# Optimization experiments

Hardware: AMD Instinct MI355X
Metric: run time of the kernel (lower is better)

The kernel has to match this reference:

```python
import jax, jax.numpy as jnp
import numpy as np

B, S, DM, H = 4, 2048, 512, 8
DEPTH = DM // H  # 64


def setup_inputs() -> dict:
    key = jax.random.key(0)
    ks = jax.random.split(key, 12)
    sd = 1.0 / np.sqrt(DM)
    return {
        "Q": jax.random.normal(ks[0], (B, S, DM), jnp.float32),
        "K": jax.random.normal(ks[1], (B, S, DM), jnp.float32),
        "V": jax.random.normal(ks[2], (B, S, DM), jnp.float32),
        "mask": jnp.zeros((B, 1, S), jnp.float32),
        "Wq": jax.random.normal(ks[3], (DM, DM), jnp.float32) * sd,
        "bq": jnp.zeros((DM,), jnp.float32),
        "Wk": jax.random.normal(ks[4], (DM, DM), jnp.float32) * sd,
        "bk": jnp.zeros((DM,), jnp.float32),
        "Wv": jax.random.normal(ks[5], (DM, DM), jnp.float32) * sd,
        "bv": jnp.zeros((DM,), jnp.float32),
        "Wo": jax.random.normal(ks[6], (DM, DM), jnp.float32) * sd,
        "bo": jnp.zeros((DM,), jnp.float32),
    }


def reference(Q, K, V, mask, Wq, bq, Wk, bk, Wv, bv, Wo, bo):
    # Linear projections to [B, S, DM]
    q = Q @ Wq + bq
    k = K @ Wk + bk
    v = V @ Wv + bv
    # Contiguous channel slices of size depth == reshape to [B, S, H, depth]
    q = q.reshape(B, S, H, DEPTH).transpose(0, 2, 1, 3)  # [B,H,S,d]
    k = k.reshape(B, S, H, DEPTH).transpose(0, 2, 1, 3)
    v = v.reshape(B, S, H, DEPTH).transpose(0, 2, 1, 3)
    scale = 1.0 / jnp.sqrt(jnp.asarray(DEPTH, q.dtype))
    scores = jnp.einsum("bhqd,bhkd->bhqk", q, k) * scale  # [B,H,S,S]
    # mask [B,1,S] broadcasts over heads and query positions
    scores = scores + mask[:, None, :, :] * -1e9
    att_ws = jax.nn.softmax(scores, axis=-1)  # [B,H,S,S]
    ctx = jnp.einsum("bhqk,bhkd->bhqd", att_ws, v)  # [B,H,S,d]
    ctx = ctx.transpose(0, 2, 1, 3).reshape(B, S, DM)  # concat heads
    Y = ctx @ Wo + bo
    return Y, att_ws
```

## Files before the change

### kernel.cpp

```cpp
#include <hip/hip_runtime.h>


typedef __bf16 bf16;
typedef __bf16 bf16x8 __attribute__((ext_vector_type(8)));
typedef float f32x4 __attribute__((ext_vector_type(4)));

constexpr int BATCH = 4;
constexpr int SEQ = 2048;
constexpr int DMODEL = 512;
constexpr int NHEAD = 8;
constexpr int HDIM = 64;
constexpr int MTOT = BATCH * SEQ;
constexpr long YELEMS = (long)MTOT * DMODEL;
constexpr long WELEMS = (long)DMODEL * DMODEL;

__device__ __forceinline__ f32x4 mfma_bf16(bf16x8 a, bf16x8 b, f32x4 c) {
  return __builtin_amdgcn_mfma_f32_16x16x32_bf16(a, b, c, 0, 0, 0);
}

__global__ void detect_k(const unsigned int* q, int* flag) {
  unsigned u = q[threadIdx.x];
  int e = (u >> 7) & 0xff;
  unsigned long long m = __ballot(e >= 0x60 && e <= 0x9f);
  if (threadIdx.x == 0) flag[0] = (__popcll(m) >= 48) ? 1 : 0;
}

__global__ void cvt_k(const void* src, bf16* dst, int n, const int* flag) {
  int i = blockIdx.x * 256 + threadIdx.x;
  if (i >= n) return;
  dst[i] = (*flag) ? ((const bf16*)src)[i] : (bf16)((const float*)src)[i];
}

__global__ __launch_bounds__(256) void transpose_w_k(const void* __restrict__ w,
                                                     bf16* __restrict__ wt,
                                                     const int* flag) {
  __shared__ bf16 t[32][33];
  const int f = *flag;
  const int bx = blockIdx.x * 32, by = blockIdx.y * 32;
  const int tx = threadIdx.x & 31, ty = threadIdx.x >> 5;
  for (int i = ty; i < 32; i += 8) {
    const long idx = (long)(by + i) * DMODEL + bx + tx;
    t[i][tx] = f ? ((const bf16*)w)[idx] : (bf16)((const float*)w)[idx];
  }
  __syncthreads();
  for (int i = ty; i < 32; i += 8)
    wt[(long)(bx + i) * DMODEL + by + tx] = t[tx][i];
}

__device__ __forceinline__ void ld8_f32(bf16* dst, const float* p) {
  float4 a = *(const float4*)p;
  float4 b = *(const float4*)(p + 4);
  bf16x8 v;
  v[0] = (bf16)a.x; v[1] = (bf16)a.y; v[2] = (bf16)a.z; v[3] = (bf16)a.w;
  v[4] = (bf16)b.x; v[5] = (bf16)b.y; v[6] = (bf16)b.z; v[7] = (bf16)b.w;
  *(bf16x8*)dst = v;
}

__global__ __launch_bounds__(256) void proj_gemm(
    const void* __restrict__ X, const bf16* __restrict__ Wt,
    const bf16* __restrict__ bias, void* __restrict__ out, int mode, int x_raw,
    const int* flag) {
  __shared__ __attribute__((aligned(16))) bf16 As[64][72];
  __shared__ __attribute__((aligned(16))) bf16 Bs[64][72];
  const int f = *flag;
  const int xf = x_raw ? f : 1;
  const int r0 = blockIdx.x * 64;
  const int c0 = blockIdx.y * 64;
  const int tid = threadIdx.x;
  const int wave = tid >> 6, lane = tid & 63;
  const int quad = lane >> 4, l16 = lane & 15;
  const int srow = tid >> 3, scb = (tid & 7) * 8;

  f32x4 acc[4] = {};
  for (int k0 = 0; k0 < DMODEL; k0 += 64) {
    __syncthreads();
    const long xi0 = (long)(r0 + srow) * DMODEL + k0 + scb;
    const long xi1 = (long)(r0 + srow + 32) * DMODEL + k0 + scb;
    if (xf) {
      *(uint4*)&As[srow][scb] = *(const uint4*)((const bf16*)X + xi0);
      *(uint4*)&As[srow + 32][scb] = *(const uint4*)((const bf16*)X + xi1);
    } else {
      ld8_f32(&As[srow][scb], (const float*)X + xi0);
      ld8_f32(&As[srow + 32][scb], (const float*)X + xi1);
    }
    *(uint4*)&Bs[srow][scb] =
        *(const uint4*)(Wt + (long)(c0 + srow) * DMODEL + k0 + scb);
    *(uint4*)&Bs[srow + 32][scb] =
        *(const uint4*)(Wt + (long)(c0 + srow + 32) * DMODEL + k0 + scb);
    __syncthreads();
    const int m = wave * 16 + l16;
#pragma unroll
    for (int kk = 0; kk < 64; kk += 32) {
      bf16x8 a = *(const bf16x8*)&As[m][kk + quad * 8];
#pragma unroll
      for (int n = 0; n < 4; n++) {
        bf16x8 bb8 = *(const bf16x8*)&Bs[n * 16 + l16][kk + quad * 8];
        acc[n] = mfma_bf16(a, bb8, acc[n]);
      }
    }
  }

  __syncthreads();
  const bool f32out = (mode == 0) && !f;
#pragma unroll
  for (int n = 0; n < 4; n++) {
    const float bvv = (float)bias[c0 + n * 16 + l16];
#pragma unroll
    for (int r = 0; r < 4; r++) {
      const float v = acc[n][r] + bvv;
      const int ml = wave * 16 + quad * 4 + r;
      const int nl = n * 16 + l16;
      if (f32out) {
        ((float*)out)[(long)(r0 + ml) * DMODEL + c0 + nl] = v;
      } else if (mode == 2) {
        As[nl][ml] = (bf16)v;
      } else {
        As[ml][nl] = (bf16)v;
      }
    }
  }
  if (f32out) return;
  __syncthreads();

  const int rb = r0 >> 11;
  const int s0 = r0 & (SEQ - 1);
  const int hh = c0 >> 6;
  bf16* ob = (bf16*)out;
#pragma unroll
  for (int i = 0; i < 2; i++) {
    const int mrow = srow + i * 32;
    long idx;
    if (mode == 0) {
      idx = (long)(r0 + mrow) * DMODEL + c0 + scb;
    } else if (mode == 1) {
      idx = (((long)(rb * NHEAD + hh) * SEQ) + s0 + mrow) * HDIM + scb;
    } else {
      idx = (((long)(rb * NHEAD + hh) * HDIM) + mrow) * SEQ + s0 + scb;
    }
    *(uint4*)(ob + idx) = *(const uint4*)&As[mrow][scb];
  }
}

__global__ __launch_bounds__(256) void attn_k(
    const bf16* __restrict__ qh, const bf16* __restrict__ kh,
    const bf16* __restrict__ vt, const bf16* __restrict__ mask_c,
    bf16* __restrict__ attB, float* __restrict__ attF, bf16* __restrict__ ctx,
    const int* flag) {
  __shared__ __attribute__((aligned(16))) bf16 qs[64][72];
  __shared__ __attribute__((aligned(16))) bf16 ks[64][72];
  __shared__ __attribute__((aligned(16))) bf16 vs[64][72];
  __shared__ __attribute__((aligned(16))) bf16 ps[64][72];
  __shared__ float mk[64];

  const int f = *flag;
  const int bh = blockIdx.y;
  const int bb = bh >> 3, hh = bh & 7;
  const int q0 = blockIdx.x * 64;
  const int tid = threadIdx.x;
  const int wave = tid >> 6, lane = tid & 63;
  const int quad = lane >> 4, l16 = lane & 15;
  const int srow = tid >> 3, scb = (tid & 7) * 8;
  const float scale = 0.125f;

  const bf16* qp = qh + ((long)bh * SEQ + q0) * HDIM;
  const bf16* kp = kh + (long)bh * SEQ * HDIM;
  const bf16* vp = vt + (long)bh * HDIM * SEQ;
  const bf16* mp = mask_c + (long)bb * SEQ;

  *(uint4*)&qs[srow][scb] = *(const uint4*)(qp + (long)srow * HDIM + scb);
  *(uint4*)&qs[srow + 32][scb] =
      *(const uint4*)(qp + (long)(srow + 32) * HDIM + scb);

  float m_ln[4], l_ln[4];
#pragma unroll
  for (int r = 0; r < 4; r++) { m_ln[r] = -3e38f; l_ln[r] = 0.f; }
  const int mrow = wave * 16 + l16;

  for (int t = 0; t < SEQ / 64; t++) {
    __syncthreads();
    const bf16* kt = kp + (long)t * 64 * HDIM;
    *(uint4*)&ks[srow][scb] = *(const uint4*)(kt + (long)srow * HDIM + scb);
    *(uint4*)&ks[srow + 32][scb] =
        *(const uint4*)(kt + (long)(srow + 32) * HDIM + scb);
    if (tid < 64) mk[tid] = -1e9f * (float)mp[t * 64 + tid];
    __syncthreads();
    f32x4 sc[4] = {};
#pragma unroll
    for (int kk = 0; kk < 64; kk += 32) {
      bf16x8 a = *(const bf16x8*)&qs[mrow][kk + quad * 8];
#pragma unroll
      for (int n = 0; n < 4; n++) {
        bf16x8 bb8 = *(const bf16x8*)&ks[n * 16 + l16][kk + quad * 8];
        sc[n] = mfma_bf16(a, bb8, sc[n]);
      }
    }
    float mv[4];
#pragma unroll
    for (int n = 0; n < 4; n++) mv[n] = mk[n * 16 + l16];
#pragma unroll
    for (int r = 0; r < 4; r++) {
      const float v0 = sc[0][r] * scale + mv[0];
      const float v1 = sc[1][r] * scale + mv[1];
      const float v2 = sc[2][r] * scale + mv[2];
      const float v3 = sc[3][r] * scale + mv[3];
      const float mx = fmaxf(fmaxf(v0, v1), fmaxf(v2, v3));
      const float mnew = fmaxf(m_ln[r], mx);
      l_ln[r] = l_ln[r] * __expf(m_ln[r] - mnew) + __expf(v0 - mnew) +
                __expf(v1 - mnew) + __expf(v2 - mnew) + __expf(v3 - mnew);
      m_ln[r] = mnew;
    }
  }

  float m_i[4], rcl[4];
#pragma unroll
  for (int r = 0; r < 4; r++) {
    float mr = m_ln[r];
#pragma unroll
    for (int o = 1; o < 16; o <<= 1) mr = fmaxf(mr, __shfl_xor(mr, o, 64));
    float lr = l_ln[r] * __expf(m_ln[r] - mr);
#pragma unroll
    for (int o = 1; o < 16; o <<= 1) lr += __shfl_xor(lr, o, 64);
    m_i[r] = mr;
    rcl[r] = 1.f / lr;
  }

  f32x4 oacc[4] = {};
  const long abase = ((long)bh * SEQ + q0) * SEQ;

  for (int t = 0; t < SEQ / 64; t++) {
    __syncthreads();
    const bf16* kt = kp + (long)t * 64 * HDIM;
    *(uint4*)&ks[srow][scb] = *(const uint4*)(kt + (long)srow * HDIM + scb);
    *(uint4*)&ks[srow + 32][scb] =
        *(const uint4*)(kt + (long)(srow + 32) * HDIM + scb);
    *(uint4*)&vs[srow][scb] =
        *(const uint4*)(vp + (long)srow * SEQ + t * 64 + scb);
    *(uint4*)&vs[srow + 32][scb] =
        *(const uint4*)(vp + (long)(srow + 32) * SEQ + t * 64 + scb);
    if (tid < 64) mk[tid] = -1e9f * (float)mp[t * 64 + tid];
    __syncthreads();
    f32x4 sc[4] = {};
#pragma unroll
    for (int kk = 0; kk < 64; kk += 32) {
      bf16x8 a = *(const bf16x8*)&qs[mrow][kk + quad * 8];
#pragma unroll
      for (int n = 0; n < 4; n++) {
        bf16x8 bb8 = *(const bf16x8*)&ks[n * 16 + l16][kk + quad * 8];
        sc[n] = mfma_bf16(a, bb8, sc[n]);
      }
    }
    float mv[4];
#pragma unroll
    for (int n = 0; n < 4; n++) mv[n] = mk[n * 16 + l16];
#pragma unroll
    for (int r = 0; r < 4; r++) {
      const int prow = wave * 16 + quad * 4 + r;
#pragma unroll
      for (int n = 0; n < 4; n++) {
        const float p = __expf(sc[n][r] * scale + mv[n] - m_i[r]) * rcl[r];
        ps[prow][n * 16 + l16] = (bf16)p;
        if (!f) attF[abase + (long)prow * SEQ + t * 64 + n * 16 + l16] = p;
      }
    }
    __syncthreads();
#pragma unroll
    for (int kk = 0; kk < 64; kk += 32) {
      bf16x8 a = *(const bf16x8*)&ps[wave * 16 + l16][kk + quad * 8];
#pragma unroll
      for (int n = 0; n < 4; n++) {
        bf16x8 bb8 = *(const bf16x8*)&vs[n * 16 + l16][kk + quad * 8];
        oacc[n] = mfma_bf16(a, bb8, oacc[n]);
      }
    }
    if (f) {
#pragma unroll
      for (int i = 0; i < 2; i++) {
        const int ci = lane + i * 64;
        const int rr = ci >> 3, cc = (ci & 7) * 8;
        *(uint4*)(attB + abase + (long)(wave * 16 + rr) * SEQ + t * 64 + cc) =
            *(const uint4*)&ps[wave * 16 + rr][cc];
      }
    }
  }

#pragma unroll
  for (int n = 0; n < 4; n++) {
#pragma unroll
    for (int r = 0; r < 4; r++) {
      const int s = q0 + wave * 16 + quad * 4 + r;
      const int d = n * 16 + l16;
      ctx[((long)bb * SEQ + s) * DMODEL + hh * HDIM + d] = (bf16)oacc[n][r];
    }
  }
}

extern "C" void kernel_launch(void* const* d_in, const int* in_sizes, int n_in,
                              void* d_out, int out_size, void* d_ws,
                              size_t ws_size, hipStream_t stream) {
  const void* Q = d_in[0];
  const void* K = d_in[1];
  const void* V = d_in[2];
  const void* mask = d_in[3];
  const void* Wq = d_in[4];
  const void* bq = d_in[5];
  const void* Wk = d_in[6];
  const void* bk = d_in[7];
  const void* Wv = d_in[8];
  const void* bv = d_in[9];
  const void* Wo = d_in[10];
  const void* bo = d_in[11];

  char* ob = (char*)d_out;
  bf16* attB = (bf16*)(ob + 2 * YELEMS);
  float* attF = (float*)(ob + 4 * YELEMS);
  bf16* qh = (bf16*)ob;

  bf16* stg = (bf16*)(ob + 4 * YELEMS);
  bf16* wqt = stg;
  bf16* wkt = wqt + WELEMS;
  bf16* wvt = wkt + WELEMS;

  char* wb = (char*)d_ws;
  int* flag = (int*)wb;
  bf16* mask_c = (bf16*)(wb + 16);
  bf16* bq_c = (bf16*)(wb + 16 + 16384);
  bf16* bk_c = bq_c + 512;
  bf16* bv_c = bk_c + 512;
  bf16* bo_c = bv_c + 512;
  bf16* kh = (bf16*)(wb + 20496);
  bf16* vtb = kh + YELEMS;
  bf16* ctx = vtb + YELEMS;
  bf16* wot = ctx + YELEMS;

  dim3 tb(256);
  detect_k<<<1, 64, 0, stream>>>((const unsigned int*)Q, flag);

  cvt_k<<<32, 256, 0, stream>>>(mask, mask_c, BATCH * SEQ, flag);
  cvt_k<<<2, 256, 0, stream>>>(bq, bq_c, DMODEL, flag);
  cvt_k<<<2, 256, 0, stream>>>(bk, bk_c, DMODEL, flag);
  cvt_k<<<2, 256, 0, stream>>>(bv, bv_c, DMODEL, flag);
  cvt_k<<<2, 256, 0, stream>>>(bo, bo_c, DMODEL, flag);

  dim3 gw(DMODEL / 32, DMODEL / 32);
  transpose_w_k<<<gw, tb, 0, stream>>>(Wq, wqt, flag);
  transpose_w_k<<<gw, tb, 0, stream>>>(Wk, wkt, flag);
  transpose_w_k<<<gw, tb, 0, stream>>>(Wv, wvt, flag);
  transpose_w_k<<<gw, tb, 0, stream>>>(Wo, wot, flag);

  dim3 gp(MTOT / 64, DMODEL / 64);
  proj_gemm<<<gp, tb, 0, stream>>>(Q, wqt, bq_c, qh, 1, 1, flag);
  proj_gemm<<<gp, tb, 0, stream>>>(K, wkt, bk_c, kh, 1, 1, flag);
  proj_gemm<<<gp, tb, 0, stream>>>(V, wvt, bv_c, vtb, 2, 1, flag);

  attn_k<<<dim3(SEQ / 64, BATCH * NHEAD), tb, 0, stream>>>(
      qh, kh, vtb, mask_c, attB, attF, ctx, flag);

  proj_gemm<<<gp, tb, 0, stream>>>(ctx, wot, bo_c, d_out, 0, 0, flag);
}
```

Before: 781.9 us.

## Batch small prep kernels, pre-convert QKV to bf16, use exp2 softmax with float mask

Merges the mask and bias conversions into one launch and the four weight transposes into one 3D-grid launch, cutting launch count. Q/K/V are converted to bf16 up front in a separate kernel so the projection GEMM always loads bf16 and drops its per-tile float conversion branch. The attention softmax now uses exp2f with log2e folded into the scale and into a precomputed float mask. Mask values are read per lane from global memory instead of through shared memory. The extra conversion pass adds a full read and write of the inputs, and the bf16 staging buffers are placed inside the output region.

```diff
diff --git a/kernel.cpp b/kernel.cpp
--- a/kernel.cpp
+++ b/kernel.cpp
@@ -13,6 +13,7 @@
 constexpr int MTOT = BATCH * SEQ;
 constexpr long YELEMS = (long)MTOT * DMODEL;
 constexpr long WELEMS = (long)DMODEL * DMODEL;
+constexpr float LOG2E = 1.44269504f;
 
 __device__ __forceinline__ f32x4 mfma_bf16(bf16x8 a, bf16x8 b, f32x4 c) {
   return __builtin_amdgcn_mfma_f32_16x16x32_bf16(a, b, c, 0, 0, 0);
@@ -25,16 +26,57 @@
   if (threadIdx.x == 0) flag[0] = (__popcll(m) >= 48) ? 1 : 0;
 }
 
-__global__ void cvt_k(const void* src, bf16* dst, int n, const int* flag) {
-  int i = blockIdx.x * 256 + threadIdx.x;
-  if (i >= n) return;
-  dst[i] = (*flag) ? ((const bf16*)src)[i] : (bf16)((const float*)src)[i];
-}
-
-__global__ __launch_bounds__(256) void transpose_w_k(const void* __restrict__ w,
-                                                     bf16* __restrict__ wt,
-                                                     const int* flag) {
+__global__ __launch_bounds__(256) void cvt_qkv_k(
+    const void* __restrict__ q, const void* __restrict__ k,
+    const void* __restrict__ v, bf16* __restrict__ qb, bf16* __restrict__ kb,
+    bf16* __restrict__ vb, const int* flag) {
+  const int z = blockIdx.y;
+  const void* src = (z == 0) ? q : (z == 1) ? k : v;
+  bf16* dst = (z == 0) ? qb : (z == 1) ? kb : vb;
+  const long i8 = ((long)blockIdx.x * 256 + threadIdx.x) * 8;
+  if (*flag) {
+    *(uint4*)(dst + i8) = *(const uint4*)((const bf16*)src + i8);
+  } else {
+    const float* s = (const float*)src + i8;
+    const float4 a = *(const float4*)s;
+    const float4 b = *(const float4*)(s + 4);
+    bf16x8 o;
+    o[0] = (bf16)a.x; o[1] = (bf16)a.y; o[2] = (bf16)a.z; o[3] = (bf16)a.w;
+    o[4] = (bf16)b.x; o[5] = (bf16)b.y; o[6] = (bf16)b.z; o[7] = (bf16)b.w;
+    *(bf16x8*)(dst + i8) = o;
+  }
+}
+
+__global__ void cvt_mb_k(const void* __restrict__ mask,
+                         const void* __restrict__ b0,
+                         const void* __restrict__ b1,
+                         const void* __restrict__ b2,
+                         const void* __restrict__ b3,
+                         float* __restrict__ maskf, bf16* __restrict__ bias_c,
+                         const int* flag) {
+  const int f = *flag;
+  const int i = blockIdx.x * 256 + threadIdx.x;
+  if (i < BATCH * SEQ) {
+    const float m = f ? (float)((const bf16*)mask)[i] : ((const float*)mask)[i];
+    maskf[i] = m * (-1e9f * LOG2E);
+  } else {
+    const int j = i - BATCH * SEQ;
+    const int w = j >> 9;
+    const void* s = (w == 0) ? b0 : (w == 1) ? b1 : (w == 2) ? b2 : b3;
+    const int o = j & 511;
+    bias_c[j] = f ? ((const bf16*)s)[o] : (bf16)((const float*)s)[o];
+  }
+}
+
+__global__ __launch_bounds__(256) void transpose_w4_k(
+    const void* __restrict__ wq, const void* __restrict__ wk,
+    const void* __restrict__ wv, const void* __restrict__ wo,
+    bf16* __restrict__ wqt, bf16* __restrict__ wkt, bf16* __restrict__ wvt,
+    bf16* __restrict__ wot, const int* flag) {
   __shared__ bf16 t[32][33];
+  const int z = blockIdx.z;
+  const void* w = (z == 0) ? wq : (z == 1) ? wk : (z == 2) ? wv : wo;
+  bf16* wt = (z == 0) ? wqt : (z == 1) ? wkt : (z == 2) ? wvt : wot;
   const int f = *flag;
   const int bx = blockIdx.x * 32, by = blockIdx.y * 32;
   const int tx = threadIdx.x & 31, ty = threadIdx.x >> 5;
@@ -47,23 +89,13 @@
     wt[(long)(bx + i) * DMODEL + by + tx] = t[tx][i];
 }
 
-__device__ __forceinline__ void ld8_f32(bf16* dst, const float* p) {
-  float4 a = *(const float4*)p;
-  float4 b = *(const float4*)(p + 4);
-  bf16x8 v;
-  v[0] = (bf16)a.x; v[1] = (bf16)a.y; v[2] = (bf16)a.z; v[3] = (bf16)a.w;
-  v[4] = (bf16)b.x; v[5] = (bf16)b.y; v[6] = (bf16)b.z; v[7] = (bf16)b.w;
-  *(bf16x8*)dst = v;
-}
-
 __global__ __launch_bounds__(256) void proj_gemm(
-    const void* __restrict__ X, const bf16* __restrict__ Wt,
-    const bf16* __restrict__ bias, void* __restrict__ out, int mode, int x_raw,
+    const bf16* __restrict__ X, const bf16* __restrict__ Wt,
+    const bf16* __restrict__ bias, void* __restrict__ out, int mode,
     const int* flag) {
   __shared__ __attribute__((aligned(16))) bf16 As[64][72];
   __shared__ __attribute__((aligned(16))) bf16 Bs[64][72];
   const int f = *flag;
-  const int xf = x_raw ? f : 1;
   const int r0 = blockIdx.x * 64;
   const int c0 = blockIdx.y * 64;
   const int tid = threadIdx.x;
@@ -74,15 +106,10 @@
   f32x4 acc[4] = {};
   for (int k0 = 0; k0 < DMODEL; k0 += 64) {
     __syncthreads();
-    const long xi0 = (long)(r0 + srow) * DMODEL + k0 + scb;
-    const long xi1 = (long)(r0 + srow + 32) * DMODEL + k0 + scb;
-    if (xf) {
-      *(uint4*)&As[srow][scb] = *(const uint4*)((const bf16*)X + xi0);
-      *(uint4*)&As[srow + 32][scb] = *(const uint4*)((const bf16*)X + xi1);
-    } else {
-      ld8_f32(&As[srow][scb], (const float*)X + xi0);
-      ld8_f32(&As[srow + 32][scb], (const float*)X + xi1);
-    }
+    *(uint4*)&As[srow][scb] =
+        *(const uint4*)(X + (long)(r0 + srow) * DMODEL + k0 + scb);
+    *(uint4*)&As[srow + 32][scb] =
+        *(const uint4*)(X + (long)(r0 + srow + 32) * DMODEL + k0 + scb);
     *(uint4*)&Bs[srow][scb] =
         *(const uint4*)(Wt + (long)(c0 + srow) * DMODEL + k0 + scb);
     *(uint4*)&Bs[srow + 32][scb] =
@@ -143,14 +170,13 @@
 
 __global__ __launch_bounds__(256) void attn_k(
     const bf16* __restrict__ qh, const bf16* __restrict__ kh,
-    const bf16* __restrict__ vt, const bf16* __restrict__ mask_c,
+    const bf16* __restrict__ vt, const float* __restrict__ maskf,
     bf16* __restrict__ attB, float* __restrict__ attF, bf16* __restrict__ ctx,
     const int* flag) {
   __shared__ __attribute__((aligned(16))) bf16 qs[64][72];
   __shared__ __attribute__((aligned(16))) bf16 ks[64][72];
   __shared__ __attribute__((aligned(16))) bf16 vs[64][72];
   __shared__ __attribute__((aligned(16))) bf16 ps[64][72];
-  __shared__ float mk[64];
 
   const int f = *flag;
   const int bh = blockIdx.y;
@@ -160,12 +186,12 @@
   const int wave = tid >> 6, lane = tid & 63;
   const int quad = lane >> 4, l16 = lane & 15;
   const int srow = tid >> 3, scb = (tid & 7) * 8;
-  const float scale = 0.125f;
+  const float scale2 = 0.125f * LOG2E;
 
   const bf16* qp = qh + ((long)bh * SEQ + q0) * HDIM;
   const bf16* kp = kh + (long)bh * SEQ * HDIM;
   const bf16* vp = vt + (long)bh * HDIM * SEQ;
-  const bf16* mp = mask_c + (long)bb * SEQ;
+  const float* mp = maskf + (long)bb * SEQ;
 
   *(uint4*)&qs[srow][scb] = *(const uint4*)(qp + (long)srow * HDIM + scb);
   *(uint4*)&qs[srow + 32][scb] =
@@ -182,7 +208,9 @@
     *(uint4*)&ks[srow][scb] = *(const uint4*)(kt + (long)srow * HDIM + scb);
     *(uint4*)&ks[srow + 32][scb] =
         *(const uint4*)(kt + (long)(srow + 32) * HDIM + scb);
-    if (tid < 64) mk[tid] = -1e9f * (float)mp[t * 64 + tid];
+    float mv[4];
+#pragma unroll
+    for (int n = 0; n < 4; n++) mv[n] = mp[t * 64 + n * 16 + l16];
     __syncthreads();
     f32x4 sc[4] = {};
 #pragma unroll
@@ -194,19 +222,16 @@
         sc[n] = mfma_bf16(a, bb8, sc[n]);
       }
     }
-    float mv[4];
-#pragma unroll
-    for (int n = 0; n < 4; n++) mv[n] = mk[n * 16 + l16];
 #pragma unroll
     for (int r = 0; r < 4; r++) {
-      const float v0 = sc[0][r] * scale + mv[0];
-      const float v1 = sc[1][r] * scale + mv[1];
-      const float v2 = sc[2][r] * scale + mv[2];
-      const float v3 = sc[3][r] * scale + mv[3];
+      const float v0 = fmaf(sc[0][r], scale2, mv[0]);
+      const float v1 = fmaf(sc[1][r], scale2, mv[1]);
+      const float v2 = fmaf(sc[2][r], scale2, mv[2]);
+      const float v3 = fmaf(sc[3][r], scale2, mv[3]);
       const float mx = fmaxf(fmaxf(v0, v1), fmaxf(v2, v3));
       const float mnew = fmaxf(m_ln[r], mx);
-      l_ln[r] = l_ln[r] * __expf(m_ln[r] - mnew) + __expf(v0 - mnew) +
-                __expf(v1 - mnew) + __expf(v2 - mnew) + __expf(v3 - mnew);
+      l_ln[r] = l_ln[r] * exp2f(m_ln[r] - mnew) + exp2f(v0 - mnew) +
+                exp2f(v1 - mnew) + exp2f(v2 - mnew) + exp2f(v3 - mnew);
       m_ln[r] = mnew;
     }
   }
@@ -217,7 +242,7 @@
     float mr = m_ln[r];
 #pragma unroll
     for (int o = 1; o < 16; o <<= 1) mr = fmaxf(mr, __shfl_xor(mr, o, 64));
-    float lr = l_ln[r] * __expf(m_ln[r] - mr);
+    float lr = l_ln[r] * exp2f(m_ln[r] - mr);
 #pragma unroll
     for (int o = 1; o < 16; o <<= 1) lr += __shfl_xor(lr, o, 64);
     m_i[r] = mr;
@@ -237,7 +262,9 @@
         *(const uint4*)(vp + (long)srow * SEQ + t * 64 + scb);
     *(uint4*)&vs[srow + 32][scb] =
         *(const uint4*)(vp + (long)(srow + 32) * SEQ + t * 64 + scb);
-    if (tid < 64) mk[tid] = -1e9f * (float)mp[t * 64 + tid];
+    float mv[4];
+#pragma unroll
+    for (int n = 0; n < 4; n++) mv[n] = mp[t * 64 + n * 16 + l16];
     __syncthreads();
     f32x4 sc[4] = {};
 #pragma unroll
@@ -249,15 +276,13 @@
         sc[n] = mfma_bf16(a, bb8, sc[n]);
       }
     }
-    float mv[4];
-#pragma unroll
-    for (int n = 0; n < 4; n++) mv[n] = mk[n * 16 + l16];
 #pragma unroll
     for (int r = 0; r < 4; r++) {
       const int prow = wave * 16 + quad * 4 + r;
 #pragma unroll
       for (int n = 0; n < 4; n++) {
-        const float p = __expf(sc[n][r] * scale + mv[n] - m_i[r]) * rcl[r];
+        const float p =
+            exp2f(fmaf(sc[n][r], scale2, mv[n]) - m_i[r]) * rcl[r];
         ps[prow][n * 16 + l16] = (bf16)p;
         if (!f) attF[abase + (long)prow * SEQ + t * 64 + n * 16 + l16] = p;
       }
@@ -319,15 +344,19 @@
   bf16* wqt = stg;
   bf16* wkt = wqt + WELEMS;
   bf16* wvt = wkt + WELEMS;
+  bf16* qb = wvt + WELEMS;
+  bf16* kb = qb + YELEMS;
+  bf16* vb = kb + YELEMS;
 
   char* wb = (char*)d_ws;
   int* flag = (int*)wb;
-  bf16* mask_c = (bf16*)(wb + 16);
-  bf16* bq_c = (bf16*)(wb + 16 + 16384);
+  float* maskf = (float*)(wb + 16);
+  bf16* bias_c = (bf16*)(wb + 16 + 32768);
+  bf16* bq_c = bias_c;
   bf16* bk_c = bq_c + 512;
   bf16* bv_c = bk_c + 512;
   bf16* bo_c = bv_c + 512;
-  bf16* kh = (bf16*)(wb + 20496);
+  bf16* kh = (bf16*)(wb + 16 + 32768 + 4096);
   bf16* vtb = kh + YELEMS;
   bf16* ctx = vtb + YELEMS;
   bf16* wot = ctx + YELEMS;
@@ -335,25 +364,19 @@
   dim3 tb(256);
   detect_k<<<1, 64, 0, stream>>>((const unsigned int*)Q, flag);
 
-  cvt_k<<<32, 256, 0, stream>>>(mask, mask_c, BATCH * SEQ, flag);
-  cvt_k<<<2, 256, 0, stream>>>(bq, bq_c, DMODEL, flag);
-  cvt_k<<<2, 256, 0, stream>>>(bk, bk_c, DMODEL, flag);
-  cvt_k<<<2, 256, 0, stream>>>(bv, bv_c, DMODEL, flag);
-  cvt_k<<<2, 256, 0, stream>>>(bo, bo_c, DMODEL, flag);
-
-  dim3 gw(DMODEL / 32, DMODEL / 32);
-  transpose_w_k<<<gw, tb, 0, stream>>>(Wq, wqt, flag);
-  transpose_w_k<<<gw, tb, 0, stream>>>(Wk, wkt, flag);
-  transpose_w_k<<<gw, tb, 0, stream>>>(Wv, wvt, flag);
-  transpose_w_k<<<gw, tb, 0, stream>>>(Wo, wot, flag);
+  cvt_mb_k<<<40, tb, 0, stream>>>(mask, bq, bk, bv, bo, maskf, bias_c, flag);
+  cvt_qkv_k<<<dim3(YELEMS / (256 * 8), 3), tb, 0, stream>>>(Q, K, V, qb, kb,
+                                                            vb, flag);
+  transpose_w4_k<<<dim3(DMODEL / 32, DMODEL / 32, 4), tb, 0, stream>>>(
+      Wq, Wk, Wv, Wo, wqt, wkt, wvt, wot, flag);
 
   dim3 gp(MTOT / 64, DMODEL / 64);
-  proj_gemm<<<gp, tb, 0, stream>>>(Q, wqt, bq_c, qh, 1, 1, flag);
-  proj_gemm<<<gp, tb, 0, stream>>>(K, wkt, bk_c, kh, 1, 1, flag);
-  proj_gemm<<<gp, tb, 0, stream>>>(V, wvt, bv_c, vtb, 2, 1, flag);
+  proj_gemm<<<gp, tb, 0, stream>>>(qb, wqt, bq_c, qh, 1, flag);
+  proj_gemm<<<gp, tb, 0, stream>>>(kb, wkt, bk_c, kh, 1, flag);
+  proj_gemm<<<gp, tb, 0, stream>>>(vb, wvt, bv_c, vtb, 2, flag);
 
   attn_k<<<dim3(SEQ / 64, BATCH * NHEAD), tb, 0, stream>>>(
-      qh, kh, vtb, mask_c, attB, attF, ctx, flag);
-
-  proj_gemm<<<gp, tb, 0, stream>>>(ctx, wot, bo_c, d_out, 0, 0, flag);
-}
+      qh, kh, vtb, maskf, attB, attF, ctx, flag);
+
+  proj_gemm<<<gp, tb, 0, stream>>>(ctx, wot, bo_c, d_out, 0, flag);
+}
```

Result: no change. 795.7 us (+1.8%).
